# Optimization experiments

Hardware: AMD Instinct MI355X
Metric: run time of the kernel (lower is better)

Reference implementation:

```python
import jax, jax.numpy as jnp
import numpy as np

N_NODES = 50000
N_EDGES = 800000
IN_CH, HID_CH, OUT_CH, HEADS = 64, 32, 64, 8
NEG_SLOPE = 0.2


def setup_inputs() -> dict:
    key = jax.random.key(0)
    ks = jax.random.split(key, 12)
    x = jax.random.normal(ks[0], (N_NODES, IN_CH), dtype=jnp.float32)
    src = jax.random.randint(ks[1], (N_EDGES,), 0, N_NODES)
    dst = jax.random.randint(ks[2], (N_EDGES,), 0, N_NODES)
    edge_index = jnp.stack([src, dst]).astype(jnp.int64)
    g1 = 1.0 / np.sqrt(IN_CH)
    g2 = 1.0 / np.sqrt(HID_CH * HEADS)
    W1 = jax.random.normal(ks[3], (IN_CH, HEADS * HID_CH), dtype=jnp.float32) * g1
    a1_src = jax.random.normal(ks[4], (HEADS, HID_CH), dtype=jnp.float32) * g1
    a1_dst = jax.random.normal(ks[5], (HEADS, HID_CH), dtype=jnp.float32) * g1
    b1 = jnp.zeros((HEADS * HID_CH,), dtype=jnp.float32)
    W2 = jax.random.normal(ks[6], (HEADS * HID_CH, OUT_CH), dtype=jnp.float32) * g2
    a2_src = jax.random.normal(ks[7], (1, OUT_CH), dtype=jnp.float32) * g2
    a2_dst = jax.random.normal(ks[8], (1, OUT_CH), dtype=jnp.float32) * g2
    b2 = jnp.zeros((OUT_CH,), dtype=jnp.float32)
    return {"x": x, "edge_index": edge_index, "W1": W1, "a1_src": a1_src,
            "a1_dst": a1_dst, "b1": b1, "W2": W2, "a2_src": a2_src,
            "a2_dst": a2_dst, "b2": b2}


def _gat_conv(x, src, dst, W, a_s, a_d, b, heads, out_ch, concat):
    """PyG GATConv: per-head linear, edge attention, segment softmax, scatter-add."""
    n = x.shape[0]
    h = (x @ W).reshape(n, heads, out_ch)                    # [N,H,C]
    al_s = jnp.einsum('nhc,hc->nh', h, a_s)                  # [N,H]
    al_d = jnp.einsum('nhc,hc->nh', h, a_d)
    e = jax.nn.leaky_relu(al_s[src] + al_d[dst], NEG_SLOPE)  # [E,H]
    m = jax.ops.segment_max(e, dst, num_segments=n)          # [N,H]
    m = jnp.where(jnp.isfinite(m), m, 0.0)
    ex = jnp.exp(e - m[dst])
    denom = jax.ops.segment_sum(ex, dst, num_segments=n)
    alpha = ex / (denom[dst] + 1e-16)                        # [E,H]
    msg = h[src] * alpha[:, :, None]                         # [E,H,C]
    out = jax.ops.segment_sum(msg, dst, num_segments=n)      # [N,H,C]
    out = out.reshape(n, heads * out_ch) if concat else out.mean(axis=1)
    return out + b


def reference(x, edge_index, W1, a1_src, a1_dst, b1, W2, a2_src, a2_dst, b2):
    n = x.shape[0]
    loops = jnp.arange(n, dtype=edge_index.dtype)
    src = jnp.concatenate([edge_index[0], loops])  # self-loops (PyG default)
    dst = jnp.concatenate([edge_index[1], loops])
    h = _gat_conv(x, src, dst, W1, a1_src, a1_dst, b1, HEADS, HID_CH, True)
    h = jax.nn.elu(h)
    return _gat_conv(h, src, dst, W2, a2_src, a2_dst, b2, 1, OUT_CH, False)
```

## Files before the change

### kernel.cpp

```cpp
#include <hip/hip_runtime.h>
#include <hip/hip_fp16.h>

#define NEG_SLOPE 0.2f
#define EPB 4096
#define CAP_B 2560

typedef unsigned int uint4v __attribute__((ext_vector_type(4)));
typedef float float4v __attribute__((ext_vector_type(4)));

__global__ __launch_bounds__(256, 4) void k_phase1(
    const int* __restrict__ ei, int E,
    const float* __restrict__ x, const float* __restrict__ W1,
    const float* __restrict__ a1s, const float* __restrict__ a1d,
    __half* __restrict__ h1h, float* __restrict__ al1s, float* __restrict__ al1d,
    int* __restrict__ cursor, unsigned* __restrict__ pairs,
    int n, int nbuck, int nP1B)
{
  __shared__ int sh[2048];
  int t = threadIdx.x;
  if (blockIdx.x < nP1B) {
    int* hist = sh;
    int* hbase = sh + 512;
    for (int i = t; i < nbuck; i += 256) hist[i] = 0;
    __syncthreads();
    int ebase = blockIdx.x * EPB;
    int pk[16], bk[16], rk[16];
#pragma unroll
    for (int k = 0; k < 16; k++) {
      int eid = ebase + k * 256 + t;
      bk[k] = -1; pk[k] = 0; rk[k] = 0;
      if (eid < E) {
        int s = ei[eid], d = ei[E + eid];
        s = (s < 0) ? 0 : (s >= n ? n - 1 : s);
        d = (d < 0) ? 0 : (d >= n ? n - 1 : d);
        bk[k] = d >> 7;
        pk[k] = ((d & 127) << 17) | s;
        rk[k] = atomicAdd(&hist[d >> 7], 1);
      }
    }
    __syncthreads();
    for (int b = t; b < nbuck; b += 256) {
      int c = hist[b];
      hbase[b] = c ? atomicAdd(&cursor[b], c) : 0;
    }
    __syncthreads();
#pragma unroll
    for (int k = 0; k < 16; k++) {
      if (bk[k] >= 0) {
        int idx = hbase[bk[k]] + rk[k];
        if (idx < CAP_B)
          pairs[(size_t)bk[k] * CAP_B + idx] = (unsigned)pk[k];
      }
    }
    return;
  }
  float (*xs)[64] = reinterpret_cast<float(*)[64]>(sh);
  int cg = t & 63;
  int mg = t >> 6;
  int base = (blockIdx.x - nP1B) * 32;
  for (int i = t; i < 32 * 16; i += 256) {
    int m = i >> 4, k4 = i & 15;
    int node = base + m;
    float4 v = make_float4(0.f, 0.f, 0.f, 0.f);
    if (node < n) v = reinterpret_cast<const float4*>(x + (size_t)node * 64)[k4];
    reinterpret_cast<float4*>(&xs[m][0])[k4] = v;
  }
  float4 as4 = reinterpret_cast<const float4*>(a1s)[cg];
  float4 ad4 = reinterpret_cast<const float4*>(a1d)[cg];
  __syncthreads();
  float4 acc[8];
#pragma unroll
  for (int m = 0; m < 8; m++) acc[m] = make_float4(0.f, 0.f, 0.f, 0.f);
#pragma unroll 1
  for (int k4 = 0; k4 < 16; k4++) {
    float4 w0 = reinterpret_cast<const float4*>(W1 + (size_t)(4 * k4 + 0) * 256)[cg];
    float4 w1 = reinterpret_cast<const float4*>(W1 + (size_t)(4 * k4 + 1) * 256)[cg];
    float4 w2 = reinterpret_cast<const float4*>(W1 + (size_t)(4 * k4 + 2) * 256)[cg];
    float4 w3 = reinterpret_cast<const float4*>(W1 + (size_t)(4 * k4 + 3) * 256)[cg];
#pragma unroll
    for (int m = 0; m < 8; m++) {
      float4 xv = reinterpret_cast<float4*>(&xs[mg * 8 + m][0])[k4];
      acc[m].x = fmaf(xv.x, w0.x, acc[m].x); acc[m].y = fmaf(xv.x, w0.y, acc[m].y);
      acc[m].z = fmaf(xv.x, w0.z, acc[m].z); acc[m].w = fmaf(xv.x, w0.w, acc[m].w);
      acc[m].x = fmaf(xv.y, w1.x, acc[m].x); acc[m].y = fmaf(xv.y, w1.y, acc[m].y);
      acc[m].z = fmaf(xv.y, w1.z, acc[m].z); acc[m].w = fmaf(xv.y, w1.w, acc[m].w);
      acc[m].x = fmaf(xv.z, w2.x, acc[m].x); acc[m].y = fmaf(xv.z, w2.y, acc[m].y);
      acc[m].z = fmaf(xv.z, w2.z, acc[m].z); acc[m].w = fmaf(xv.z, w2.w, acc[m].w);
      acc[m].x = fmaf(xv.w, w3.x, acc[m].x); acc[m].y = fmaf(xv.w, w3.y, acc[m].y);
      acc[m].z = fmaf(xv.w, w3.z, acc[m].z); acc[m].w = fmaf(xv.w, w3.w, acc[m].w);
    }
  }
#pragma unroll
  for (int m = 0; m < 8; m++) {
    int node = base + mg * 8 + m;
    if (node < n) {
      int head = cg >> 3;
      __half2 p01 = __floats2half2_rn(acc[m].x, acc[m].y);
      __half2 p23 = __floats2half2_rn(acc[m].z, acc[m].w);
      uint2 pko;
      pko.x = *reinterpret_cast<unsigned int*>(&p01);
      pko.y = *reinterpret_cast<unsigned int*>(&p23);
      reinterpret_cast<uint2*>(h1h + (size_t)head * n * 32 + (size_t)node * 32)[cg & 7] = pko;
      float s_ = acc[m].x * as4.x + acc[m].y * as4.y + acc[m].z * as4.z + acc[m].w * as4.w;
      float d_ = acc[m].x * ad4.x + acc[m].y * ad4.y + acc[m].z * ad4.z + acc[m].w * ad4.w;
      s_ += __shfl_xor(s_, 1); d_ += __shfl_xor(d_, 1);
      s_ += __shfl_xor(s_, 2); d_ += __shfl_xor(d_, 2);
      s_ += __shfl_xor(s_, 4); d_ += __shfl_xor(d_, 4);
      if ((cg & 7) == 0) {
        al1s[(size_t)head * n + node] = s_;
        al1d[(size_t)head * n + node] = d_;
      }
    }
  }
}

__global__ __launch_bounds__(256) void k_pass2(
    const unsigned* __restrict__ pairs, const int* __restrict__ cursor,
    int* __restrict__ gcur, int* __restrict__ deg, int* __restrict__ rowoff,
    int* __restrict__ csr, int n)
{
  __shared__ int cnt[128], off[128], rk[128];
  __shared__ int bbase;
  int b = blockIdx.x, t = threadIdx.x;
  if (t < 128) { cnt[t] = 0; rk[t] = 0; }
  __syncthreads();
  int total = min(cursor[b], CAP_B);
  size_t base = (size_t)b * CAP_B;
  for (int i = t; i < total; i += 256)
    atomicAdd(&cnt[pairs[base + i] >> 17], 1);
  __syncthreads();
  if (t == 0) {
    int run = 0;
    for (int i = 0; i < 128; i++) { off[i] = run; run += cnt[i]; }
    bbase = atomicAdd(gcur, run);
  }
  __syncthreads();
  int bb = bbase;
  if (t < 128) {
    int node = (b << 7) + t;
    if (node < n) { deg[node] = cnt[t]; rowoff[node] = bb + off[t]; }
  }
  for (int i = t; i < total; i += 256) {
    unsigned p = pairs[base + i];
    int local = p >> 17;
    int slot = atomicAdd(&rk[local], 1);
    csr[bb + off[local] + slot] = (int)(p & 0x1FFFF);
  }
}

__global__ __launch_bounds__(256, 4) void k_linear2(
    const __half* __restrict__ hacth, const float* __restrict__ W2,
    const float* __restrict__ a2s, const float* __restrict__ a2d,
    __half* __restrict__ h2h, float* __restrict__ al2s, float* __restrict__ al2d,
    int n)
{
  __shared__ float xs[32][260];
  int t = threadIdx.x;
  int cg = t & 15;
  int mg = t >> 4;
  int base = blockIdx.x * 32;
  for (int i = t; i < 32 * 32; i += 256) {
    int m = i >> 5, c8 = i & 31;
    int node = base + m;
    uint4 pk = make_uint4(0, 0, 0, 0);
    if (node < n) pk = reinterpret_cast<const uint4*>(hacth + (size_t)node * 256)[c8];
    __half2* hp = reinterpret_cast<__half2*>(&pk);
    float2 f0 = __half22float2(hp[0]);
    float2 f1 = __half22float2(hp[1]);
    float2 f2 = __half22float2(hp[2]);
    float2 f3 = __half22float2(hp[3]);
    float4* dst = reinterpret_cast<float4*>(&xs[m][c8 * 8]);
    dst[0] = make_float4(f0.x, f0.y, f1.x, f1.y);
    dst[1] = make_float4(f2.x, f2.y, f3.x, f3.y);
  }
  float4 as4 = reinterpret_cast<const float4*>(a2s)[cg];
  float4 ad4 = reinterpret_cast<const float4*>(a2d)[cg];
  __syncthreads();
  float4 a0 = make_float4(0.f, 0.f, 0.f, 0.f);
  float4 a1 = make_float4(0.f, 0.f, 0.f, 0.f);
#pragma unroll 2
  for (int k4 = 0; k4 < 64; k4++) {
    float4 w0 = reinterpret_cast<const float4*>(W2 + (size_t)(4 * k4 + 0) * 64)[cg];
    float4 w1 = reinterpret_cast<const float4*>(W2 + (size_t)(4 * k4 + 1) * 64)[cg];
    float4 w2 = reinterpret_cast<const float4*>(W2 + (size_t)(4 * k4 + 2) * 64)[cg];
    float4 w3 = reinterpret_cast<const float4*>(W2 + (size_t)(4 * k4 + 3) * 64)[cg];
    float4 x0 = *reinterpret_cast<float4*>(&xs[2 * mg + 0][k4 * 4]);
    float4 x1 = *reinterpret_cast<float4*>(&xs[2 * mg + 1][k4 * 4]);
    a0.x = fmaf(x0.x, w0.x, a0.x); a0.y = fmaf(x0.x, w0.y, a0.y);
    a0.z = fmaf(x0.x, w0.z, a0.z); a0.w = fmaf(x0.x, w0.w, a0.w);
    a0.x = fmaf(x0.y, w1.x, a0.x); a0.y = fmaf(x0.y, w1.y, a0.y);
    a0.z = fmaf(x0.y, w1.z, a0.z); a0.w = fmaf(x0.y, w1.w, a0.w);
    a0.x = fmaf(x0.z, w2.x, a0.x); a0.y = fmaf(x0.z, w2.y, a0.y);
    a0.z = fmaf(x0.z, w2.z, a0.z); a0.w = fmaf(x0.z, w2.w, a0.w);
    a0.x = fmaf(x0.w, w3.x, a0.x); a0.y = fmaf(x0.w, w3.y, a0.y);
    a0.z = fmaf(x0.w, w3.z, a0.z); a0.w = fmaf(x0.w, w3.w, a0.w);
    a1.x = fmaf(x1.x, w0.x, a1.x); a1.y = fmaf(x1.x, w0.y, a1.y);
    a1.z = fmaf(x1.x, w0.z, a1.z); a1.w = fmaf(x1.x, w0.w, a1.w);
    a1.x = fmaf(x1.y, w1.x, a1.x); a1.y = fmaf(x1.y, w1.y, a1.y);
    a1.z = fmaf(x1.y, w1.z, a1.z); a1.w = fmaf(x1.y, w1.w, a1.w);
    a1.x = fmaf(x1.z, w2.x, a1.x); a1.y = fmaf(x1.z, w2.y, a1.y);
    a1.z = fmaf(x1.z, w2.z, a1.z); a1.w = fmaf(x1.z, w2.w, a1.w);
    a1.x = fmaf(x1.w, w3.x, a1.x); a1.y = fmaf(x1.w, w3.y, a1.y);
    a1.z = fmaf(x1.w, w3.z, a1.z); a1.w = fmaf(x1.w, w3.w, a1.w);
  }
#pragma unroll
  for (int nd = 0; nd < 2; nd++) {
    float4 a = nd ? a1 : a0;
    int node = base + 2 * mg + nd;
    if (node < n) {
      __half2 q0 = __floats2half2_rn(a.x, a.y);
      __half2 q1 = __floats2half2_rn(a.z, a.w);
      uint2 pk;
      pk.x = *reinterpret_cast<unsigned int*>(&q0);
      pk.y = *reinterpret_cast<unsigned int*>(&q1);
      reinterpret_cast<uint2*>(h2h + (size_t)(cg >> 3) * n * 32 + (size_t)node * 32)[cg & 7] = pk;
      float s_ = a.x * as4.x + a.y * as4.y + a.z * as4.z + a.w * as4.w;
      float d_ = a.x * ad4.x + a.y * ad4.y + a.z * ad4.z + a.w * ad4.w;
      s_ += __shfl_xor(s_, 1); d_ += __shfl_xor(d_, 1);
      s_ += __shfl_xor(s_, 2); d_ += __shfl_xor(d_, 2);
      s_ += __shfl_xor(s_, 4); d_ += __shfl_xor(d_, 4);
      s_ += __shfl_xor(s_, 8); d_ += __shfl_xor(d_, 8);
      if (cg == 0) { al2s[node] = s_; al2d[node] = d_; }
    }
  }
}

__global__ __launch_bounds__(256) void k_gather1(
    const __half* __restrict__ h1h, const float* __restrict__ al1s, const float* __restrict__ al1d,
    const int* __restrict__ degv, const int* __restrict__ rowoff, const int* __restrict__ csr,
    const float* __restrict__ b1, __half* __restrict__ hacth, int n)
{
  int head = blockIdx.x & 7;
  int node = ((blockIdx.x >> 3) << 6) + (threadIdx.x >> 2);
  if (node >= n) return;
  int q = threadIdx.x & 3;
  const __half* slab = h1h + (size_t)head * n * 32;
  const float* als = al1s + (size_t)head * n;
  float ald = al1d[(size_t)head * n + node];
  int beg = rowoff[node];
  int deg = degv[node];
  uint4 nr = reinterpret_cast<const uint4*>(slab + (size_t)node * 32)[q];
  float eS = als[node] + ald;
  eS = eS > 0.f ? eS : NEG_SLOPE * eS;
  float exS = __expf(eS);
  float acc[8];
#pragma unroll
  for (int k = 0; k < 8; k++) acc[k] = 0.f;
  float den = 0.f;
  if (deg > 0) {
    int s0 = csr[beg];
    int s1 = (deg > 1) ? csr[beg + 1] : 0;
    int s2 = (deg > 2) ? csr[beg + 2] : 0;
    float alA = als[s0];
    uint4 pA = reinterpret_cast<const uint4*>(slab + (size_t)s0 * 32)[q];
    float alB = 0.f;
    uint4 pB = make_uint4(0, 0, 0, 0);
    if (deg > 1) {
      alB = als[s1];
      pB = reinterpret_cast<const uint4*>(slab + (size_t)s1 * 32)[q];
    }
    for (int i = 0; i < deg; i++) {
      float alC = 0.f;
      uint4 pC = make_uint4(0, 0, 0, 0);
      if (i + 2 < deg) {
        alC = als[s2];
        pC = reinterpret_cast<const uint4*>(slab + (size_t)s2 * 32)[q];
      }
      int s3 = (i + 3 < deg) ? csr[beg + i + 3] : 0;
      float e = alA + ald;
      e = e > 0.f ? e : NEG_SLOPE * e;
      float ex = __expf(e);
      den += ex;
      __half2* hp = reinterpret_cast<__half2*>(&pA);
#pragma unroll
      for (int j = 0; j < 4; j++) {
        float2 f = __half22float2(hp[j]);
        acc[2 * j + 0] = fmaf(ex, f.x, acc[2 * j + 0]);
        acc[2 * j + 1] = fmaf(ex, f.y, acc[2 * j + 1]);
      }
      alA = alB; pA = pB; alB = alC; pB = pC; s2 = s3;
    }
  }
  den += exS;
  {
    __half2* hp = reinterpret_cast<__half2*>(&nr);
#pragma unroll
    for (int j = 0; j < 4; j++) {
      float2 f = __half22float2(hp[j]);
      acc[2 * j + 0] = fmaf(exS, f.x, acc[2 * j + 0]);
      acc[2 * j + 1] = fmaf(exS, f.y, acc[2 * j + 1]);
    }
  }
  float inv = 1.f / (den + 1e-16f);
  const float4* bb = reinterpret_cast<const float4*>(b1 + head * 32);
  float4 b40 = bb[2 * q], b41 = bb[2 * q + 1];
  float o[8];
  o[0] = acc[0] * inv + b40.x; o[1] = acc[1] * inv + b40.y;
  o[2] = acc[2] * inv + b40.z; o[3] = acc[3] * inv + b40.w;
  o[4] = acc[4] * inv + b41.x; o[5] = acc[5] * inv + b41.y;
  o[6] = acc[6] * inv + b41.z; o[7] = acc[7] * inv + b41.w;
#pragma unroll
  for (int k = 0; k < 8; k++) o[k] = o[k] > 0.f ? o[k] : (__expf(o[k]) - 1.f);
  uint4v w0;
  __half2 t0, t1;
  t0 = __floats2half2_rn(o[0], o[1]);  w0.x = *reinterpret_cast<unsigned int*>(&t0);
  t1 = __floats2half2_rn(o[2], o[3]);  w0.y = *reinterpret_cast<unsigned int*>(&t1);
  t0 = __floats2half2_rn(o[4], o[5]);  w0.z = *reinterpret_cast<unsigned int*>(&t0);
  t1 = __floats2half2_rn(o[6], o[7]);  w0.w = *reinterpret_cast<unsigned int*>(&t1);
  __builtin_nontemporal_store(
      w0, reinterpret_cast<uint4v*>(hacth + (size_t)node * 256 + head * 32 + q * 8));
}

__global__ __launch_bounds__(256) void k_gather2(
    const __half* __restrict__ h2h, const float* __restrict__ al2s, const float* __restrict__ al2d,
    const int* __restrict__ degv, const int* __restrict__ rowoff, const int* __restrict__ csr,
    const float* __restrict__ b2, float* __restrict__ out, int n)
{
  int c = blockIdx.x & 1;
  int node = ((blockIdx.x >> 1) << 6) + (threadIdx.x >> 2);
  if (node >= n) return;
  int q = threadIdx.x & 3;
  const __half* slab = h2h + (size_t)c * n * 32;
  float ald = al2d[node];
  int beg = rowoff[node];
  int deg = degv[node];
  uint4 nr = reinterpret_cast<const uint4*>(slab + (size_t)node * 32)[q];
  float eS = al2s[node] + ald;
  eS = eS > 0.f ? eS : NEG_SLOPE * eS;
  float exS = __expf(eS);
  float acc[8];
#pragma unroll
  for (int k = 0; k < 8; k++) acc[k] = 0.f;
  float den = 0.f;
  if (deg > 0) {
    int s0 = csr[beg];
    int s1 = (deg > 1) ? csr[beg + 1] : 0;
    int s2 = (deg > 2) ? csr[beg + 2] : 0;
    float alA = al2s[s0];
    uint4 pA = reinterpret_cast<const uint4*>(slab + (size_t)s0 * 32)[q];
    float alB = 0.f;
    uint4 pB = make_uint4(0, 0, 0, 0);
    if (deg > 1) {
      alB = al2s[s1];
      pB = reinterpret_cast<const uint4*>(slab + (size_t)s1 * 32)[q];
    }
    for (int i = 0; i < deg; i++) {
      float alC = 0.f;
      uint4 pC = make_uint4(0, 0, 0, 0);
      if (i + 2 < deg) {
        alC = al2s[s2];
        pC = reinterpret_cast<const uint4*>(slab + (size_t)s2 * 32)[q];
      }
      int s3 = (i + 3 < deg) ? csr[beg + i + 3] : 0;
      float e = alA + ald;
      e = e > 0.f ? e : NEG_SLOPE * e;
      float ex = __expf(e);
      den += ex;
      __half2* hp = reinterpret_cast<__half2*>(&pA);
#pragma unroll
      for (int j = 0; j < 4; j++) {
        float2 f = __half22float2(hp[j]);
        acc[2 * j + 0] = fmaf(ex, f.x, acc[2 * j + 0]);
        acc[2 * j + 1] = fmaf(ex, f.y, acc[2 * j + 1]);
      }
      alA = alB; pA = pB; alB = alC; pB = pC; s2 = s3;
    }
  }
  den += exS;
  {
    __half2* hp = reinterpret_cast<__half2*>(&nr);
#pragma unroll
    for (int j = 0; j < 4; j++) {
      float2 f = __half22float2(hp[j]);
      acc[2 * j + 0] = fmaf(exS, f.x, acc[2 * j + 0]);
      acc[2 * j + 1] = fmaf(exS, f.y, acc[2 * j + 1]);
    }
  }
  float inv = 1.f / (den + 1e-16f);
  const float4* bb = reinterpret_cast<const float4*>(b2 + c * 32);
  float4 b40 = bb[2 * q], b41 = bb[2 * q + 1];
  float* op = out + (size_t)node * 64 + c * 32 + q * 8;
  float4v o0, o1;
  o0.x = acc[0] * inv + b40.x; o0.y = acc[1] * inv + b40.y;
  o0.z = acc[2] * inv + b40.z; o0.w = acc[3] * inv + b40.w;
  o1.x = acc[4] * inv + b41.x; o1.y = acc[5] * inv + b41.y;
  o1.z = acc[6] * inv + b41.z; o1.w = acc[7] * inv + b41.w;
  __builtin_nontemporal_store(o0, reinterpret_cast<float4v*>(op));
  __builtin_nontemporal_store(o1, reinterpret_cast<float4v*>(op) + 1);
}

extern "C" void kernel_launch(void* const* d_in, const int* in_sizes, int n_in,
                              void* d_out, int out_size, void* d_ws, size_t ws_size,
                              hipStream_t stream)
{
  const float* x        = (const float*)d_in[0];
  const int*   ei       = (const int*)d_in[1];
  const float* W1       = (const float*)d_in[2];
  const float* a1s      = (const float*)d_in[3];
  const float* a1d      = (const float*)d_in[4];
  const float* b1       = (const float*)d_in[5];
  const float* W2       = (const float*)d_in[6];
  const float* a2s      = (const float*)d_in[7];
  const float* a2d      = (const float*)d_in[8];
  const float* b2       = (const float*)d_in[9];
  float* out            = (float*)d_out;

  int N  = in_sizes[0] / 64;
  int E  = in_sizes[1] / 2;
  int NBUCK = (N + 127) >> 7;

  char* p = (char*)d_ws;
  auto alloc = [&](size_t bytes) -> char* {
    char* r = p;
    p += (bytes + 255) & ~(size_t)255;
    return r;
  };
  __half* h1h    = (__half*)alloc((size_t)N * 256 * 2);
  __half* hacth  = (__half*)alloc((size_t)N * 256 * 2);
  float* al1s    = (float*)alloc((size_t)N * 8 * 4);
  float* al1d    = (float*)alloc((size_t)N * 8 * 4);
  float* al2s    = (float*)alloc((size_t)N * 4);
  float* al2d    = (float*)alloc((size_t)N * 4);
  int*   deg     = (int*)alloc((size_t)N * 4);
  int*   rowoff  = (int*)alloc((size_t)N * 4);
  int*   csr     = (int*)alloc((size_t)NBUCK * CAP_B * 4);
  unsigned* pairs = (unsigned*)alloc((size_t)NBUCK * CAP_B * 4);
  int*   cursor  = (int*)alloc((size_t)(NBUCK + 1) * 4);
  int*   gcur    = cursor + NBUCK;
  __half* h2h    = h1h;

  hipMemsetAsync(cursor, 0, (size_t)(NBUCK + 1) * 4, stream);

  int nP1B = (E + EPB - 1) / EPB;
  int nLB = (N + 31) / 32;
  k_phase1<<<nP1B + nLB, 256, 0, stream>>>(ei, E, x, W1, a1s, a1d,
                                           h1h, al1s, al1d, cursor, pairs, N, NBUCK, nP1B);
  k_pass2<<<NBUCK, 256, 0, stream>>>(pairs, cursor, gcur, deg, rowoff, csr, N);
  int nG1 = 8 * ((N + 63) / 64);
  k_gather1<<<nG1, 256, 0, stream>>>(h1h, al1s, al1d, deg, rowoff, csr, b1, hacth, N);
  k_linear2<<<(N + 31) / 32, 256, 0, stream>>>(hacth, W2, a2s, a2d, h2h, al2s, al2d, N);
  int nG2 = 2 * ((N + 63) / 64);
  k_gather2<<<nG2, 256, 0, stream>>>(h2h, al2s, al2d, deg, rowoff, csr, b2, out, N);
}
```

Baseline: 221.7 us.

## Sort nodes by degree within buckets and gather neighbors two at a time

The CSR build now pads each row to an even length, writing a zero-index pad entry, and emits a per-bucket node order sorted by in-degree, capped at 64. Both gather kernels read their node through this order, so wavefronts handle nodes of similar degree and lose less time to lanes idling on short rows. The gather loops now load two neighbor indices at once as an int2 and double-buffer two neighbors per step, which increases memory-level parallelism. The cost is an extra indirection through the order array, scattered output writes, and a wasted padded load for odd degrees.

New measurement: 234.6 us. +5.8%, slower.

```diff
diff --git a/kernel.cpp b/kernel.cpp
--- a/kernel.cpp
+++ b/kernel.cpp
@@ -117,12 +117,13 @@
 __global__ __launch_bounds__(256) void k_pass2(
     const unsigned* __restrict__ pairs, const int* __restrict__ cursor,
     int* __restrict__ gcur, int* __restrict__ deg, int* __restrict__ rowoff,
-    int* __restrict__ csr, int n)
-{
-  __shared__ int cnt[128], off[128], rk[128];
+    int* __restrict__ csr, int* __restrict__ order, int n)
+{
+  __shared__ int cnt[128], off[128], rk[128], dh[68];
   __shared__ int bbase;
   int b = blockIdx.x, t = threadIdx.x;
   if (t < 128) { cnt[t] = 0; rk[t] = 0; }
+  if (t >= 128 && t < 196) dh[t - 128] = 0;
   __syncthreads();
   int total = min(cursor[b], CAP_B);
   size_t base = (size_t)b * CAP_B;
@@ -131,14 +132,31 @@
   __syncthreads();
   if (t == 0) {
     int run = 0;
-    for (int i = 0; i < 128; i++) { off[i] = run; run += cnt[i]; }
+    for (int i = 0; i < 128; i++) { off[i] = run; run += (cnt[i] + 1) & ~1; }
     bbase = atomicAdd(gcur, run);
   }
   __syncthreads();
   int bb = bbase;
+  int key = 66;
   if (t < 128) {
     int node = (b << 7) + t;
-    if (node < n) { deg[node] = cnt[t]; rowoff[node] = bb + off[t]; }
+    if (node < n) {
+      deg[node] = cnt[t];
+      rowoff[node] = bb + off[t];
+      if (cnt[t] & 1) csr[bb + off[t] + cnt[t]] = 0;
+      key = min(cnt[t], 64);
+    } else key = 65;
+    atomicAdd(&dh[key], 1);
+  }
+  __syncthreads();
+  if (t == 0) {
+    int r = 0;
+    for (int i = 0; i < 66; i++) { int c = dh[i]; dh[i] = r; r += c; }
+  }
+  __syncthreads();
+  if (t < 128) {
+    int rank = atomicAdd(&dh[key], 1);
+    order[(b << 7) + rank] = (b << 7) + t;
   }
   for (int i = t; i < total; i += 256) {
     unsigned p = pairs[base + i];
@@ -225,13 +243,42 @@
   }
 }
 
+#define G_LOAD(tt, sv, a0v, a1v, q0v, q1v, ALT)                                 \
+  {                                                                             \
+    sv = *reinterpret_cast<const int2*>(csr + beg + 2 * (tt));                  \
+    a0v = ALT[sv.x]; a1v = ALT[sv.y];                                           \
+    q0v = reinterpret_cast<const uint4*>(slab)[4 * sv.x + q];                   \
+    q1v = reinterpret_cast<const uint4*>(slab)[4 * sv.y + q];                   \
+  }
+#define G_COMPUTE(a0v, a1v, q0v, q1v, tt)                                       \
+  {                                                                             \
+    float e0 = a0v + ald; e0 = e0 > 0.f ? e0 : NEG_SLOPE * e0;                  \
+    float e1 = a1v + ald; e1 = e1 > 0.f ? e1 : NEG_SLOPE * e1;                  \
+    float x0 = __expf(e0);                                                      \
+    float x1 = (2 * (tt) + 1 < deg) ? __expf(e1) : 0.f;                         \
+    den += x0 + x1;                                                             \
+    __half2* h0 = reinterpret_cast<__half2*>(&q0v);                             \
+    __half2* h1 = reinterpret_cast<__half2*>(&q1v);                             \
+    _Pragma("unroll")                                                           \
+    for (int j = 0; j < 4; j++) {                                               \
+      float2 f0 = __half22float2(h0[j]);                                        \
+      float2 f1 = __half22float2(h1[j]);                                        \
+      acc[2 * j + 0] = fmaf(x0, f0.x, acc[2 * j + 0]);                          \
+      acc[2 * j + 1] = fmaf(x0, f0.y, acc[2 * j + 1]);                          \
+      acc[2 * j + 0] = fmaf(x1, f1.x, acc[2 * j + 0]);                          \
+      acc[2 * j + 1] = fmaf(x1, f1.y, acc[2 * j + 1]);                          \
+    }                                                                           \
+  }
+
 __global__ __launch_bounds__(256) void k_gather1(
     const __half* __restrict__ h1h, const float* __restrict__ al1s, const float* __restrict__ al1d,
     const int* __restrict__ degv, const int* __restrict__ rowoff, const int* __restrict__ csr,
-    const float* __restrict__ b1, __half* __restrict__ hacth, int n)
+    const int* __restrict__ order, const float* __restrict__ b1,
+    __half* __restrict__ hacth, int n)
 {
   int head = blockIdx.x & 7;
-  int node = ((blockIdx.x >> 3) << 6) + (threadIdx.x >> 2);
+  int slot = ((blockIdx.x >> 3) << 6) + (threadIdx.x >> 2);
+  int node = order[slot];
   if (node >= n) return;
   int q = threadIdx.x & 3;
   const __half* slab = h1h + (size_t)head * n * 32;
@@ -239,7 +286,7 @@
   float ald = al1d[(size_t)head * n + node];
   int beg = rowoff[node];
   int deg = degv[node];
-  uint4 nr = reinterpret_cast<const uint4*>(slab + (size_t)node * 32)[q];
+  uint4 nr = reinterpret_cast<const uint4*>(slab)[4 * node + q];
   float eS = als[node] + ald;
   eS = eS > 0.f ? eS : NEG_SLOPE * eS;
   float exS = __expf(eS);
@@ -247,38 +294,20 @@
 #pragma unroll
   for (int k = 0; k < 8; k++) acc[k] = 0.f;
   float den = 0.f;
-  if (deg > 0) {
-    int s0 = csr[beg];
-    int s1 = (deg > 1) ? csr[beg + 1] : 0;
-    int s2 = (deg > 2) ? csr[beg + 2] : 0;
-    float alA = als[s0];
-    uint4 pA = reinterpret_cast<const uint4*>(slab + (size_t)s0 * 32)[q];
-    float alB = 0.f;
-    uint4 pB = make_uint4(0, 0, 0, 0);
-    if (deg > 1) {
-      alB = als[s1];
-      pB = reinterpret_cast<const uint4*>(slab + (size_t)s1 * 32)[q];
-    }
-    for (int i = 0; i < deg; i++) {
-      float alC = 0.f;
-      uint4 pC = make_uint4(0, 0, 0, 0);
-      if (i + 2 < deg) {
-        alC = als[s2];
-        pC = reinterpret_cast<const uint4*>(slab + (size_t)s2 * 32)[q];
-      }
-      int s3 = (i + 3 < deg) ? csr[beg + i + 3] : 0;
-      float e = alA + ald;
-      e = e > 0.f ? e : NEG_SLOPE * e;
-      float ex = __expf(e);
-      den += ex;
-      __half2* hp = reinterpret_cast<__half2*>(&pA);
-#pragma unroll
-      for (int j = 0; j < 4; j++) {
-        float2 f = __half22float2(hp[j]);
-        acc[2 * j + 0] = fmaf(ex, f.x, acc[2 * j + 0]);
-        acc[2 * j + 1] = fmaf(ex, f.y, acc[2 * j + 1]);
-      }
-      alA = alB; pA = pB; alB = alC; pB = pC; s2 = s3;
+  int nt = (deg + 1) >> 1;
+  if (nt > 0) {
+    int2 sA, sB;
+    float aA0, aA1, aB0, aB1;
+    uint4 qA0, qA1, qB0, qB1;
+    G_LOAD(0, sA, aA0, aA1, qA0, qA1, als);
+    int t2 = 0;
+    while (true) {
+      if (t2 + 1 < nt) G_LOAD(t2 + 1, sB, aB0, aB1, qB0, qB1, als);
+      G_COMPUTE(aA0, aA1, qA0, qA1, t2);
+      if (++t2 >= nt) break;
+      if (t2 + 1 < nt) G_LOAD(t2 + 1, sA, aA0, aA1, qA0, qA1, als);
+      G_COMPUTE(aB0, aB1, qB0, qB1, t2);
+      if (++t2 >= nt) break;
     }
   }
   den += exS;
@@ -314,17 +343,19 @@
 __global__ __launch_bounds__(256) void k_gather2(
     const __half* __restrict__ h2h, const float* __restrict__ al2s, const float* __restrict__ al2d,
     const int* __restrict__ degv, const int* __restrict__ rowoff, const int* __restrict__ csr,
-    const float* __restrict__ b2, float* __restrict__ out, int n)
+    const int* __restrict__ order, const float* __restrict__ b2,
+    float* __restrict__ out, int n)
 {
   int c = blockIdx.x & 1;
-  int node = ((blockIdx.x >> 1) << 6) + (threadIdx.x >> 2);
+  int slot = ((blockIdx.x >> 1) << 6) + (threadIdx.x >> 2);
+  int node = order[slot];
   if (node >= n) return;
   int q = threadIdx.x & 3;
   const __half* slab = h2h + (size_t)c * n * 32;
   float ald = al2d[node];
   int beg = rowoff[node];
   int deg = degv[node];
-  uint4 nr = reinterpret_cast<const uint4*>(slab + (size_t)node * 32)[q];
+  uint4 nr = reinterpret_cast<const uint4*>(slab)[4 * node + q];
   float eS = al2s[node] + ald;
   eS = eS > 0.f ? eS : NEG_SLOPE * eS;
   float exS = __expf(eS);
@@ -332,38 +363,20 @@
 #pragma unroll
   for (int k = 0; k < 8; k++) acc[k] = 0.f;
   float den = 0.f;
-  if (deg > 0) {
-    int s0 = csr[beg];
-    int s1 = (deg > 1) ? csr[beg + 1] : 0;
-    int s2 = (deg > 2) ? csr[beg + 2] : 0;
-    float alA = al2s[s0];
-    uint4 pA = reinterpret_cast<const uint4*>(slab + (size_t)s0 * 32)[q];
-    float alB = 0.f;
-    uint4 pB = make_uint4(0, 0, 0, 0);
-    if (deg > 1) {
-      alB = al2s[s1];
-      pB = reinterpret_cast<const uint4*>(slab + (size_t)s1 * 32)[q];
-    }
-    for (int i = 0; i < deg; i++) {
-      float alC = 0.f;
-      uint4 pC = make_uint4(0, 0, 0, 0);
-      if (i + 2 < deg) {
-        alC = al2s[s2];
-        pC = reinterpret_cast<const uint4*>(slab + (size_t)s2 * 32)[q];
-      }
-      int s3 = (i + 3 < deg) ? csr[beg + i + 3] : 0;
-      float e = alA + ald;
-      e = e > 0.f ? e : NEG_SLOPE * e;
-      float ex = __expf(e);
-      den += ex;
-      __half2* hp = reinterpret_cast<__half2*>(&pA);
-#pragma unroll
-      for (int j = 0; j < 4; j++) {
-        float2 f = __half22float2(hp[j]);
-        acc[2 * j + 0] = fmaf(ex, f.x, acc[2 * j + 0]);
-        acc[2 * j + 1] = fmaf(ex, f.y, acc[2 * j + 1]);
-      }
-      alA = alB; pA = pB; alB = alC; pB = pC; s2 = s3;
+  int nt = (deg + 1) >> 1;
+  if (nt > 0) {
+    int2 sA, sB;
+    float aA0, aA1, aB0, aB1;
+    uint4 qA0, qA1, qB0, qB1;
+    G_LOAD(0, sA, aA0, aA1, qA0, qA1, al2s);
+    int t2 = 0;
+    while (true) {
+      if (t2 + 1 < nt) G_LOAD(t2 + 1, sB, aB0, aB1, qB0, qB1, al2s);
+      G_COMPUTE(aA0, aA1, qA0, qA1, t2);
+      if (++t2 >= nt) break;
+      if (t2 + 1 < nt) G_LOAD(t2 + 1, sA, aA0, aA1, qA0, qA1, al2s);
+      G_COMPUTE(aB0, aB1, qB0, qB1, t2);
+      if (++t2 >= nt) break;
     }
   }
   den += exS;
@@ -423,6 +436,7 @@
   float* al2d    = (float*)alloc((size_t)N * 4);
   int*   deg     = (int*)alloc((size_t)N * 4);
   int*   rowoff  = (int*)alloc((size_t)N * 4);
+  int*   order   = (int*)alloc((size_t)NBUCK * 128 * 4);
   int*   csr     = (int*)alloc((size_t)NBUCK * CAP_B * 4);
   unsigned* pairs = (unsigned*)alloc((size_t)NBUCK * CAP_B * 4);
   int*   cursor  = (int*)alloc((size_t)(NBUCK + 1) * 4);
@@ -435,10 +449,10 @@
   int nLB = (N + 31) / 32;
   k_phase1<<<nP1B + nLB, 256, 0, stream>>>(ei, E, x, W1, a1s, a1d,
                                            h1h, al1s, al1d, cursor, pairs, N, NBUCK, nP1B);
-  k_pass2<<<NBUCK, 256, 0, stream>>>(pairs, cursor, gcur, deg, rowoff, csr, N);
+  k_pass2<<<NBUCK, 256, 0, stream>>>(pairs, cursor, gcur, deg, rowoff, csr, order, N);
   int nG1 = 8 * ((N + 63) / 64);
-  k_gather1<<<nG1, 256, 0, stream>>>(h1h, al1s, al1d, deg, rowoff, csr, b1, hacth, N);
+  k_gather1<<<nG1, 256, 0, stream>>>(h1h, al1s, al1d, deg, rowoff, csr, order, b1, hacth, N);
   k_linear2<<<(N + 31) / 32, 256, 0, stream>>>(hacth, W2, a2s, a2d, h2h, al2s, al2d, N);
   int nG2 = 2 * ((N + 63) / 64);
-  k_gather2<<<nG2, 256, 0, stream>>>(h2h, al2s, al2d, deg, rowoff, csr, b2, out, N);
-}
+  k_gather2<<<nG2, 256, 0, stream>>>(h2h, al2s, al2d, deg, rowoff, csr, order, b2, out, N);
+}
```

## Split layer-1 gather across four edge lanes with padded CSR rows

Applied to the files above, without the earlier changes.

Gather1 now assigns 8 threads per node-head: four lanes process interleaved edges while two halves cover 16 channels each, then partial sums are combined with cross-lane shuffles. CSR rows are padded to multiples of four with dummy indices masked out, so each lane can stride through edges uniformly. This aims to raise memory-level parallelism for the irregular neighbor loads, at the cost of shuffle reductions, wasted padded lanes, and doubled grid size.

After: 217.9 us. Within noise of the previous version (-1.7%).

```diff
diff --git a/kernel.cpp b/kernel.cpp
--- a/kernel.cpp
+++ b/kernel.cpp
@@ -131,14 +131,19 @@
   __syncthreads();
   if (t == 0) {
     int run = 0;
-    for (int i = 0; i < 128; i++) { off[i] = run; run += cnt[i]; }
+    for (int i = 0; i < 128; i++) { off[i] = run; run += (cnt[i] + 3) & ~3; }
     bbase = atomicAdd(gcur, run);
   }
   __syncthreads();
   int bb = bbase;
   if (t < 128) {
     int node = (b << 7) + t;
-    if (node < n) { deg[node] = cnt[t]; rowoff[node] = bb + off[t]; }
+    if (node < n) {
+      deg[node] = cnt[t];
+      rowoff[node] = bb + off[t];
+      int padded = (cnt[t] + 3) & ~3;
+      for (int pp = cnt[t]; pp < padded; pp++) csr[bb + off[t] + pp] = 0;
+    }
   }
   for (int i = t; i < total; i += 256) {
     unsigned p = pairs[base + i];
@@ -231,84 +236,108 @@
     const float* __restrict__ b1, __half* __restrict__ hacth, int n)
 {
   int head = blockIdx.x & 7;
-  int node = ((blockIdx.x >> 3) << 6) + (threadIdx.x >> 2);
+  int node = (blockIdx.x >> 3) * 32 + (threadIdx.x >> 3);
   if (node >= n) return;
-  int q = threadIdx.x & 3;
-  const __half* slab = h1h + (size_t)head * n * 32;
+  int r = threadIdx.x & 7;
+  int h = r & 1;
+  int o = r >> 1;
+  const uint4* slab4 = reinterpret_cast<const uint4*>(h1h + (size_t)head * n * 32);
   const float* als = al1s + (size_t)head * n;
   float ald = al1d[(size_t)head * n + node];
   int beg = rowoff[node];
   int deg = degv[node];
-  uint4 nr = reinterpret_cast<const uint4*>(slab + (size_t)node * 32)[q];
+  float acc[16];
+#pragma unroll
+  for (int k = 0; k < 16; k++) acc[k] = 0.f;
+  float den = 0.f;
+  int nt4 = (deg + 3) >> 2;
+  if (nt4 > 0) {
+    int idx = o;
+    int sA = csr[beg + idx];
+    float alA = als[sA];
+    uint4 a0 = slab4[4 * sA + 2 * h], a1 = slab4[4 * sA + 2 * h + 1];
+    bool mA = idx < deg;
+    for (int it = 0; it < nt4; it++) {
+      int idxB = idx + 4;
+      float alB = 0.f;
+      uint4 b0 = make_uint4(0, 0, 0, 0), b1v = make_uint4(0, 0, 0, 0);
+      bool mB = false;
+      if (it + 1 < nt4) {
+        int sB = csr[beg + idxB];
+        alB = als[sB];
+        b0 = slab4[4 * sB + 2 * h]; b1v = slab4[4 * sB + 2 * h + 1];
+        mB = idxB < deg;
+      }
+      float e = alA + ald;
+      e = e > 0.f ? e : NEG_SLOPE * e;
+      float ex = mA ? __expf(e) : 0.f;
+      den += ex;
+      __half2* hp0 = reinterpret_cast<__half2*>(&a0);
+      __half2* hp1 = reinterpret_cast<__half2*>(&a1);
+#pragma unroll
+      for (int j = 0; j < 4; j++) {
+        float2 f0 = __half22float2(hp0[j]);
+        float2 f1 = __half22float2(hp1[j]);
+        acc[2 * j + 0] = fmaf(ex, f0.x, acc[2 * j + 0]);
+        acc[2 * j + 1] = fmaf(ex, f0.y, acc[2 * j + 1]);
+        acc[8 + 2 * j + 0] = fmaf(ex, f1.x, acc[8 + 2 * j + 0]);
+        acc[8 + 2 * j + 1] = fmaf(ex, f1.y, acc[8 + 2 * j + 1]);
+      }
+      alA = alB; a0 = b0; a1 = b1v; mA = mB; idx = idxB;
+    }
+  }
+  den += __shfl_xor(den, 2);
+  den += __shfl_xor(den, 4);
+#pragma unroll
+  for (int k = 0; k < 16; k++) {
+    acc[k] += __shfl_xor(acc[k], 2);
+    acc[k] += __shfl_xor(acc[k], 4);
+  }
   float eS = als[node] + ald;
   eS = eS > 0.f ? eS : NEG_SLOPE * eS;
   float exS = __expf(eS);
-  float acc[8];
-#pragma unroll
-  for (int k = 0; k < 8; k++) acc[k] = 0.f;
-  float den = 0.f;
-  if (deg > 0) {
-    int s0 = csr[beg];
-    int s1 = (deg > 1) ? csr[beg + 1] : 0;
-    int s2 = (deg > 2) ? csr[beg + 2] : 0;
-    float alA = als[s0];
-    uint4 pA = reinterpret_cast<const uint4*>(slab + (size_t)s0 * 32)[q];
-    float alB = 0.f;
-    uint4 pB = make_uint4(0, 0, 0, 0);
-    if (deg > 1) {
-      alB = als[s1];
-      pB = reinterpret_cast<const uint4*>(slab + (size_t)s1 * 32)[q];
-    }
-    for (int i = 0; i < deg; i++) {
-      float alC = 0.f;
-      uint4 pC = make_uint4(0, 0, 0, 0);
-      if (i + 2 < deg) {
-        alC = als[s2];
-        pC = reinterpret_cast<const uint4*>(slab + (size_t)s2 * 32)[q];
-      }
-      int s3 = (i + 3 < deg) ? csr[beg + i + 3] : 0;
-      float e = alA + ald;
-      e = e > 0.f ? e : NEG_SLOPE * e;
-      float ex = __expf(e);
-      den += ex;
-      __half2* hp = reinterpret_cast<__half2*>(&pA);
-#pragma unroll
-      for (int j = 0; j < 4; j++) {
-        float2 f = __half22float2(hp[j]);
-        acc[2 * j + 0] = fmaf(ex, f.x, acc[2 * j + 0]);
-        acc[2 * j + 1] = fmaf(ex, f.y, acc[2 * j + 1]);
-      }
-      alA = alB; pA = pB; alB = alC; pB = pC; s2 = s3;
-    }
-  }
   den += exS;
   {
-    __half2* hp = reinterpret_cast<__half2*>(&nr);
+    uint4 n0 = slab4[4 * node + 2 * h], n1 = slab4[4 * node + 2 * h + 1];
+    __half2* hp0 = reinterpret_cast<__half2*>(&n0);
+    __half2* hp1 = reinterpret_cast<__half2*>(&n1);
 #pragma unroll
     for (int j = 0; j < 4; j++) {
-      float2 f = __half22float2(hp[j]);
-      acc[2 * j + 0] = fmaf(exS, f.x, acc[2 * j + 0]);
-      acc[2 * j + 1] = fmaf(exS, f.y, acc[2 * j + 1]);
-    }
-  }
+      float2 f0 = __half22float2(hp0[j]);
+      float2 f1 = __half22float2(hp1[j]);
+      acc[2 * j + 0] = fmaf(exS, f0.x, acc[2 * j + 0]);
+      acc[2 * j + 1] = fmaf(exS, f0.y, acc[2 * j + 1]);
+      acc[8 + 2 * j + 0] = fmaf(exS, f1.x, acc[8 + 2 * j + 0]);
+      acc[8 + 2 * j + 1] = fmaf(exS, f1.y, acc[8 + 2 * j + 1]);
+    }
+  }
+  if (o != 0) return;
   float inv = 1.f / (den + 1e-16f);
   const float4* bb = reinterpret_cast<const float4*>(b1 + head * 32);
-  float4 b40 = bb[2 * q], b41 = bb[2 * q + 1];
-  float o[8];
-  o[0] = acc[0] * inv + b40.x; o[1] = acc[1] * inv + b40.y;
-  o[2] = acc[2] * inv + b40.z; o[3] = acc[3] * inv + b40.w;
-  o[4] = acc[4] * inv + b41.x; o[5] = acc[5] * inv + b41.y;
-  o[6] = acc[6] * inv + b41.z; o[7] = acc[7] * inv + b41.w;
-#pragma unroll
-  for (int k = 0; k < 8; k++) o[k] = o[k] > 0.f ? o[k] : (__expf(o[k]) - 1.f);
-  uint4v w0;
+  float ov[16];
+#pragma unroll
+  for (int j = 0; j < 4; j++) {
+    float4 b4 = bb[4 * h + j];
+    ov[4 * j + 0] = acc[4 * j + 0] * inv + b4.x;
+    ov[4 * j + 1] = acc[4 * j + 1] * inv + b4.y;
+    ov[4 * j + 2] = acc[4 * j + 2] * inv + b4.z;
+    ov[4 * j + 3] = acc[4 * j + 3] * inv + b4.w;
+  }
+#pragma unroll
+  for (int k = 0; k < 16; k++) ov[k] = ov[k] > 0.f ? ov[k] : (__expf(ov[k]) - 1.f);
+  uint4v w0, w1;
   __half2 t0, t1;
-  t0 = __floats2half2_rn(o[0], o[1]);  w0.x = *reinterpret_cast<unsigned int*>(&t0);
-  t1 = __floats2half2_rn(o[2], o[3]);  w0.y = *reinterpret_cast<unsigned int*>(&t1);
-  t0 = __floats2half2_rn(o[4], o[5]);  w0.z = *reinterpret_cast<unsigned int*>(&t0);
-  t1 = __floats2half2_rn(o[6], o[7]);  w0.w = *reinterpret_cast<unsigned int*>(&t1);
-  __builtin_nontemporal_store(
-      w0, reinterpret_cast<uint4v*>(hacth + (size_t)node * 256 + head * 32 + q * 8));
+  t0 = __floats2half2_rn(ov[0], ov[1]);   w0.x = *reinterpret_cast<unsigned int*>(&t0);
+  t1 = __floats2half2_rn(ov[2], ov[3]);   w0.y = *reinterpret_cast<unsigned int*>(&t1);
+  t0 = __floats2half2_rn(ov[4], ov[5]);   w0.z = *reinterpret_cast<unsigned int*>(&t0);
+  t1 = __floats2half2_rn(ov[6], ov[7]);   w0.w = *reinterpret_cast<unsigned int*>(&t1);
+  t0 = __floats2half2_rn(ov[8], ov[9]);   w1.x = *reinterpret_cast<unsigned int*>(&t0);
+  t1 = __floats2half2_rn(ov[10], ov[11]); w1.y = *reinterpret_cast<unsigned int*>(&t1);
+  t0 = __floats2half2_rn(ov[12], ov[13]); w1.z = *reinterpret_cast<unsigned int*>(&t0);
+  t1 = __floats2half2_rn(ov[14], ov[15]); w1.w = *reinterpret_cast<unsigned int*>(&t1);
+  uint4v* orow = reinterpret_cast<uint4v*>(hacth + (size_t)node * 256 + head * 32 + h * 16);
+  __builtin_nontemporal_store(w0, orow);
+  __builtin_nontemporal_store(w1, orow + 1);
 }
 
 __global__ __launch_bounds__(256) void k_gather2(
@@ -436,7 +465,7 @@
   k_phase1<<<nP1B + nLB, 256, 0, stream>>>(ei, E, x, W1, a1s, a1d,
                                            h1h, al1s, al1d, cursor, pairs, N, NBUCK, nP1B);
   k_pass2<<<NBUCK, 256, 0, stream>>>(pairs, cursor, gcur, deg, rowoff, csr, N);
-  int nG1 = 8 * ((N + 63) / 64);
+  int nG1 = 8 * ((N + 31) / 32);
   k_gather1<<<nG1, 256, 0, stream>>>(h1h, al1s, al1d, deg, rowoff, csr, b1, hacth, N);
   k_linear2<<<(N + 31) / 32, 256, 0, stream>>>(hacth, W2, a2s, a2d, h2h, al2s, al2d, N);
   int nG2 = 2 * ((N + 63) / 64);
```

## Split each node's neighbor list across four lanes in gather kernels

Applied to the files above, without the earlier changes.

The gather kernels now use 16 threads per node instead of 4. Four sub-groups each walk every fourth neighbor, and their partial sums are combined with cross-lane shuffles. The CSR rows are padded to a multiple of four with zero indices so the strided loop needs no bounds check on the index load; padded slots contribute zero weight. This adds memory-level parallelism on the latency-bound gathers and shortens the serial per-node dependency chain. The costs are more threads, reduction shuffles, larger CSR offsets, and wasted loads on padded entries.

Result: faster. 207.0 us (-6.6%).

```diff
diff --git a/kernel.cpp b/kernel.cpp
--- a/kernel.cpp
+++ b/kernel.cpp
@@ -131,14 +131,19 @@
   __syncthreads();
   if (t == 0) {
     int run = 0;
-    for (int i = 0; i < 128; i++) { off[i] = run; run += cnt[i]; }
+    for (int i = 0; i < 128; i++) { off[i] = run; run += (cnt[i] + 3) & ~3; }
     bbase = atomicAdd(gcur, run);
   }
   __syncthreads();
   int bb = bbase;
   if (t < 128) {
     int node = (b << 7) + t;
-    if (node < n) { deg[node] = cnt[t]; rowoff[node] = bb + off[t]; }
+    if (node < n) {
+      deg[node] = cnt[t];
+      rowoff[node] = bb + off[t];
+      int padded = (cnt[t] + 3) & ~3;
+      for (int pp = cnt[t]; pp < padded; pp++) csr[bb + off[t] + pp] = 0;
+    }
   }
   for (int i = t; i < total; i += 256) {
     unsigned p = pairs[base + i];
@@ -231,58 +236,52 @@
     const float* __restrict__ b1, __half* __restrict__ hacth, int n)
 {
   int head = blockIdx.x & 7;
-  int node = ((blockIdx.x >> 3) << 6) + (threadIdx.x >> 2);
+  int node = (blockIdx.x >> 3) * 16 + (threadIdx.x >> 4);
   if (node >= n) return;
-  int q = threadIdx.x & 3;
-  const __half* slab = h1h + (size_t)head * n * 32;
+  int r = threadIdx.x & 15;
+  int o = r >> 2;
+  int qq = r & 3;
+  const uint4* slab4 = reinterpret_cast<const uint4*>(h1h + (size_t)head * n * 32);
   const float* als = al1s + (size_t)head * n;
   float ald = al1d[(size_t)head * n + node];
   int beg = rowoff[node];
   int deg = degv[node];
-  uint4 nr = reinterpret_cast<const uint4*>(slab + (size_t)node * 32)[q];
+  float acc[8];
+#pragma unroll
+  for (int k = 0; k < 8; k++) acc[k] = 0.f;
+  float den = 0.f;
+  int nt4 = (deg + 3) >> 2;
+#pragma unroll 2
+  for (int it = 0; it < nt4; it++) {
+    int idx = 4 * it + o;
+    int s = csr[beg + idx];
+    float al = als[s];
+    uint4 pv = slab4[4 * (size_t)s + qq];
+    float e = al + ald;
+    e = e > 0.f ? e : NEG_SLOPE * e;
+    float ex = (idx < deg) ? __expf(e) : 0.f;
+    den += ex;
+    __half2* hp = reinterpret_cast<__half2*>(&pv);
+#pragma unroll
+    for (int j = 0; j < 4; j++) {
+      float2 f = __half22float2(hp[j]);
+      acc[2 * j + 0] = fmaf(ex, f.x, acc[2 * j + 0]);
+      acc[2 * j + 1] = fmaf(ex, f.y, acc[2 * j + 1]);
+    }
+  }
+  den += __shfl_xor(den, 4);
+  den += __shfl_xor(den, 8);
+#pragma unroll
+  for (int k = 0; k < 8; k++) {
+    acc[k] += __shfl_xor(acc[k], 4);
+    acc[k] += __shfl_xor(acc[k], 8);
+  }
   float eS = als[node] + ald;
   eS = eS > 0.f ? eS : NEG_SLOPE * eS;
   float exS = __expf(eS);
-  float acc[8];
-#pragma unroll
-  for (int k = 0; k < 8; k++) acc[k] = 0.f;
-  float den = 0.f;
-  if (deg > 0) {
-    int s0 = csr[beg];
-    int s1 = (deg > 1) ? csr[beg + 1] : 0;
-    int s2 = (deg > 2) ? csr[beg + 2] : 0;
-    float alA = als[s0];
-    uint4 pA = reinterpret_cast<const uint4*>(slab + (size_t)s0 * 32)[q];
-    float alB = 0.f;
-    uint4 pB = make_uint4(0, 0, 0, 0);
-    if (deg > 1) {
-      alB = als[s1];
-      pB = reinterpret_cast<const uint4*>(slab + (size_t)s1 * 32)[q];
-    }
-    for (int i = 0; i < deg; i++) {
-      float alC = 0.f;
-      uint4 pC = make_uint4(0, 0, 0, 0);
-      if (i + 2 < deg) {
-        alC = als[s2];
-        pC = reinterpret_cast<const uint4*>(slab + (size_t)s2 * 32)[q];
-      }
-      int s3 = (i + 3 < deg) ? csr[beg + i + 3] : 0;
-      float e = alA + ald;
-      e = e > 0.f ? e : NEG_SLOPE * e;
-      float ex = __expf(e);
-      den += ex;
-      __half2* hp = reinterpret_cast<__half2*>(&pA);
-#pragma unroll
-      for (int j = 0; j < 4; j++) {
-        float2 f = __half22float2(hp[j]);
-        acc[2 * j + 0] = fmaf(ex, f.x, acc[2 * j + 0]);
-        acc[2 * j + 1] = fmaf(ex, f.y, acc[2 * j + 1]);
-      }
-      alA = alB; pA = pB; alB = alC; pB = pC; s2 = s3;
-    }
-  }
   den += exS;
   {
+    uint4 nr = slab4[4 * (size_t)node + qq];
     __half2* hp = reinterpret_cast<__half2*>(&nr);
 #pragma unroll
     for (int j = 0; j < 4; j++) {
@@ -291,24 +290,25 @@
       acc[2 * j + 1] = fmaf(exS, f.y, acc[2 * j + 1]);
     }
   }
+  if (o != 0) return;
   float inv = 1.f / (den + 1e-16f);
   const float4* bb = reinterpret_cast<const float4*>(b1 + head * 32);
-  float4 b40 = bb[2 * q], b41 = bb[2 * q + 1];
-  float o[8];
-  o[0] = acc[0] * inv + b40.x; o[1] = acc[1] * inv + b40.y;
-  o[2] = acc[2] * inv + b40.z; o[3] = acc[3] * inv + b40.w;
-  o[4] = acc[4] * inv + b41.x; o[5] = acc[5] * inv + b41.y;
-  o[6] = acc[6] * inv + b41.z; o[7] = acc[7] * inv + b41.w;
-#pragma unroll
-  for (int k = 0; k < 8; k++) o[k] = o[k] > 0.f ? o[k] : (__expf(o[k]) - 1.f);
+  float4 b40 = bb[2 * qq], b41 = bb[2 * qq + 1];
+  float ov[8];
+  ov[0] = acc[0] * inv + b40.x; ov[1] = acc[1] * inv + b40.y;
+  ov[2] = acc[2] * inv + b40.z; ov[3] = acc[3] * inv + b40.w;
+  ov[4] = acc[4] * inv + b41.x; ov[5] = acc[5] * inv + b41.y;
+  ov[6] = acc[6] * inv + b41.z; ov[7] = acc[7] * inv + b41.w;
+#pragma unroll
+  for (int k = 0; k < 8; k++) ov[k] = ov[k] > 0.f ? ov[k] : (__expf(ov[k]) - 1.f);
   uint4v w0;
   __half2 t0, t1;
-  t0 = __floats2half2_rn(o[0], o[1]);  w0.x = *reinterpret_cast<unsigned int*>(&t0);
-  t1 = __floats2half2_rn(o[2], o[3]);  w0.y = *reinterpret_cast<unsigned int*>(&t1);
-  t0 = __floats2half2_rn(o[4], o[5]);  w0.z = *reinterpret_cast<unsigned int*>(&t0);
-  t1 = __floats2half2_rn(o[6], o[7]);  w0.w = *reinterpret_cast<unsigned int*>(&t1);
+  t0 = __floats2half2_rn(ov[0], ov[1]);  w0.x = *reinterpret_cast<unsigned int*>(&t0);
+  t1 = __floats2half2_rn(ov[2], ov[3]);  w0.y = *reinterpret_cast<unsigned int*>(&t1);
+  t0 = __floats2half2_rn(ov[4], ov[5]);  w0.z = *reinterpret_cast<unsigned int*>(&t0);
+  t1 = __floats2half2_rn(ov[6], ov[7]);  w0.w = *reinterpret_cast<unsigned int*>(&t1);
   __builtin_nontemporal_store(
-      w0, reinterpret_cast<uint4v*>(hacth + (size_t)node * 256 + head * 32 + q * 8));
+      w0, reinterpret_cast<uint4v*>(hacth + (size_t)node * 256 + head * 32 + qq * 8));
 }
 
 __global__ __launch_bounds__(256) void k_gather2(
@@ -317,57 +317,51 @@
     const float* __restrict__ b2, float* __restrict__ out, int n)
 {
   int c = blockIdx.x & 1;
-  int node = ((blockIdx.x >> 1) << 6) + (threadIdx.x >> 2);
+  int node = (blockIdx.x >> 1) * 16 + (threadIdx.x >> 4);
   if (node >= n) return;
-  int q = threadIdx.x & 3;
-  const __half* slab = h2h + (size_t)c * n * 32;
+  int r = threadIdx.x & 15;
+  int o = r >> 2;
+  int qq = r & 3;
+  const uint4* slab4 = reinterpret_cast<const uint4*>(h2h + (size_t)c * n * 32);
   float ald = al2d[node];
   int beg = rowoff[node];
   int deg = degv[node];
-  uint4 nr = reinterpret_cast<const uint4*>(slab + (size_t)node * 32)[q];
+  float acc[8];
+#pragma unroll
+  for (int k = 0; k < 8; k++) acc[k] = 0.f;
+  float den = 0.f;
+  int nt4 = (deg + 3) >> 2;
+#pragma unroll 2
+  for (int it = 0; it < nt4; it++) {
+    int idx = 4 * it + o;
+    int s = csr[beg + idx];
+    float al = al2s[s];
+    uint4 pv = slab4[4 * (size_t)s + qq];
+    float e = al + ald;
+    e = e > 0.f ? e : NEG_SLOPE * e;
+    float ex = (idx < deg) ? __expf(e) : 0.f;
+    den += ex;
+    __half2* hp = reinterpret_cast<__half2*>(&pv);
+#pragma unroll
+    for (int j = 0; j < 4; j++) {
+      float2 f = __half22float2(hp[j]);
+      acc[2 * j + 0] = fmaf(ex, f.x, acc[2 * j + 0]);
+      acc[2 * j + 1] = fmaf(ex, f.y, acc[2 * j + 1]);
+    }
+  }
+  den += __shfl_xor(den, 4);
+  den += __shfl_xor(den, 8);
+#pragma unroll
+  for (int k = 0; k < 8; k++) {
+    acc[k] += __shfl_xor(acc[k], 4);
+    acc[k] += __shfl_xor(acc[k], 8);
+  }
   float eS = al2s[node] + ald;
   eS = eS > 0.f ? eS : NEG_SLOPE * eS;
   float exS = __expf(eS);
-  float acc[8];
-#pragma unroll
-  for (int k = 0; k < 8; k++) acc[k] = 0.f;
-  float den = 0.f;
-  if (deg > 0) {
-    int s0 = csr[beg];
-    int s1 = (deg > 1) ? csr[beg + 1] : 0;
-    int s2 = (deg > 2) ? csr[beg + 2] : 0;
-    float alA = al2s[s0];
-    uint4 pA = reinterpret_cast<const uint4*>(slab + (size_t)s0 * 32)[q];
-    float alB = 0.f;
-    uint4 pB = make_uint4(0, 0, 0, 0);
-    if (deg > 1) {
-      alB = al2s[s1];
-      pB = reinterpret_cast<const uint4*>(slab + (size_t)s1 * 32)[q];
-    }
-    for (int i = 0; i < deg; i++) {
-      float alC = 0.f;
-      uint4 pC = make_uint4(0, 0, 0, 0);
-      if (i + 2 < deg) {
-        alC = al2s[s2];
-        pC = reinterpret_cast<const uint4*>(slab + (size_t)s2 * 32)[q];
-      }
-      int s3 = (i + 3 < deg) ? csr[beg + i + 3] : 0;
-      float e = alA + ald;
-      e = e > 0.f ? e : NEG_SLOPE * e;
-      float ex = __expf(e);
-      den += ex;
-      __half2* hp = reinterpret_cast<__half2*>(&pA);
-#pragma unroll
-      for (int j = 0; j < 4; j++) {
-        float2 f = __half22float2(hp[j]);
-        acc[2 * j + 0] = fmaf(ex, f.x, acc[2 * j + 0]);
-        acc[2 * j + 1] = fmaf(ex, f.y, acc[2 * j + 1]);
-      }
-      alA = alB; pA = pB; alB = alC; pB = pC; s2 = s3;
-    }
-  }
   den += exS;
   {
+    uint4 nr = slab4[4 * (size_t)node + qq];
     __half2* hp = reinterpret_cast<__half2*>(&nr);
 #pragma unroll
     for (int j = 0; j < 4; j++) {
@@ -376,10 +370,11 @@
       acc[2 * j + 1] = fmaf(exS, f.y, acc[2 * j + 1]);
     }
   }
+  if (o != 0) return;
   float inv = 1.f / (den + 1e-16f);
   const float4* bb = reinterpret_cast<const float4*>(b2 + c * 32);
-  float4 b40 = bb[2 * q], b41 = bb[2 * q + 1];
-  float* op = out + (size_t)node * 64 + c * 32 + q * 8;
+  float4 b40 = bb[2 * qq], b41 = bb[2 * qq + 1];
+  float* op = out + (size_t)node * 64 + c * 32 + qq * 8;
   float4v o0, o1;
   o0.x = acc[0] * inv + b40.x; o0.y = acc[1] * inv + b40.y;
   o0.z = acc[2] * inv + b40.z; o0.w = acc[3] * inv + b40.w;
@@ -436,9 +431,9 @@
   k_phase1<<<nP1B + nLB, 256, 0, stream>>>(ei, E, x, W1, a1s, a1d,
                                            h1h, al1s, al1d, cursor, pairs, N, NBUCK, nP1B);
   k_pass2<<<NBUCK, 256, 0, stream>>>(pairs, cursor, gcur, deg, rowoff, csr, N);
-  int nG1 = 8 * ((N + 63) / 64);
+  int nG1 = 8 * ((N + 15) / 16);
   k_gather1<<<nG1, 256, 0, stream>>>(h1h, al1s, al1d, deg, rowoff, csr, b1, hacth, N);
   k_linear2<<<(N + 31) / 32, 256, 0, stream>>>(hacth, W2, a2s, a2d, h2h, al2s, al2d, N);
-  int nG2 = 2 * ((N + 63) / 64);
+  int nG2 = 2 * ((N + 15) / 16);
   k_gather2<<<nG2, 256, 0, stream>>>(h2h, al2s, al2d, deg, rowoff, csr, b2, out, N);
 }
```
